# Kernel optimization log

Measured on AMD Instinct MI355X. Metric: run time of the kernel, lower is better.

The kernel has to match this reference:

```python
import jax, jax.numpy as jnp
import numpy as np

B, N, D = 8, 64, 512          # batch, latent tokens, token dim
C, H, W, P = 256, 128, 128, 36  # img feat channels/HW, sampling points
PG = 128                       # parameter-generator inner dim (0.25*D)
HEADS = 8                      # D // 64
TOT = C * C + P * P            # adaptive mixing param count per token


def _ln(x, g, b):
    m = x.mean(-1, keepdims=True)
    v = x.var(-1, keepdims=True)
    return (x - m) / jnp.sqrt(v + 1e-5) * g + b


def _gelu(x):
    return jax.nn.gelu(x, approximate=False)


def _grid_sample(img, grid):
    # img: (B,C,H,W); grid: (B,N,P,2) in [-1,1]; bilinear, border pad, align_corners=False
    Bi, Ci, Hi, Wi = img.shape
    x = ((grid[..., 0] + 1.0) * Wi - 1.0) * 0.5
    y = ((grid[..., 1] + 1.0) * Hi - 1.0) * 0.5
    x0 = jnp.floor(x)
    y0 = jnp.floor(y)
    wx = x - x0
    wy = y - y0
    x0i = jnp.clip(x0.astype(jnp.int32), 0, Wi - 1)
    x1i = jnp.clip(x0.astype(jnp.int32) + 1, 0, Wi - 1)
    y0i = jnp.clip(y0.astype(jnp.int32), 0, Hi - 1)
    y1i = jnp.clip(y0.astype(jnp.int32) + 1, 0, Hi - 1)
    imgt = img.transpose(0, 2, 3, 1)  # (B,H,W,C)
    bidx = jnp.arange(Bi)[:, None, None]
    v00 = imgt[bidx, y0i, x0i]  # (B,N,P,C)
    v01 = imgt[bidx, y0i, x1i]
    v10 = imgt[bidx, y1i, x0i]
    v11 = imgt[bidx, y1i, x1i]
    wx = wx[..., None]
    wy = wy[..., None]
    return (v00 * (1 - wx) * (1 - wy) + v01 * wx * (1 - wy)
            + v10 * (1 - wx) * wy + v11 * wx * wy)


def setup_inputs() -> dict:
    key = jax.random.key(0)
    ks = jax.random.split(key, 16)
    rn = lambda k, s, sc: jax.random.normal(k, s, jnp.float32) * sc
    tl = jax.random.uniform(ks[0], (B, N, 2), jnp.float32) * 0.5
    wh = 0.2 + jax.random.uniform(ks[1], (B, N, 2), jnp.float32) * 0.4
    return dict(
        token_embed=rn(ks[2], (B, N, D), 1.0),
        token_roi=jnp.concatenate([tl, tl + wh], axis=-1),
        img_feat=rn(ks[3], (B, C, H, W), 1.0),
        ln_off_g=jnp.ones(D), ln_off_b=jnp.zeros(D),
        w_off=rn(ks[4], (D, P * 2), D ** -0.5),
        roi_offset_bias=rn(ks[5], (P * 2,), 1.0),
        ln_pg_g=jnp.ones(D), ln_pg_b=jnp.zeros(D),
        w_pg1=rn(ks[6], (D, PG), D ** -0.5), b_pg1=jnp.zeros(PG),
        w_pg2=rn(ks[7], (PG, TOT), 0.02 * PG ** -0.5),
        b_pg2=rn(ks[8], (TOT,), 0.02),
        m_beta=jnp.zeros(C), s_beta=jnp.zeros(P),
        w_out=rn(ks[9], (P * C, D), (P * C) ** -0.5), b_out=jnp.zeros(D),
        ln1_g=jnp.ones(D), ln1_b=jnp.zeros(D),
        w_qkv=rn(ks[10], (D, 3 * D), D ** -0.5), b_qkv=jnp.zeros(3 * D),
        w_proj=rn(ks[11], (D, D), D ** -0.5), b_proj=jnp.zeros(D),
        ln2_g=jnp.ones(D), ln2_b=jnp.zeros(D),
        w_fc1=rn(ks[12], (D, 4 * D), D ** -0.5), b_fc1=jnp.zeros(4 * D),
        w_fc2=rn(ks[13], (4 * D, D), (4 * D) ** -0.5), b_fc2=jnp.zeros(D),
    )


def reference(token_embed, token_roi, img_feat,
              ln_off_g, ln_off_b, w_off, roi_offset_bias,
              ln_pg_g, ln_pg_b, w_pg1, b_pg1, w_pg2, b_pg2,
              m_beta, s_beta, w_out, b_out,
              ln1_g, ln1_b, w_qkv, b_qkv, w_proj, b_proj,
              ln2_g, ln2_b, w_fc1, b_fc1, w_fc2, b_fc2):
    Bq, Nq, Dm = token_embed.shape
    # --- OP.SAMPLING_M: offsets -> absolute points (n_heads=1) ---
    off = _ln(token_embed, ln_off_g, ln_off_b) @ w_off + roi_offset_bias  # (B,N,2P)
    off = off.reshape(Bq, Nq, 1, P, 2)
    mu = off.mean(-2, keepdims=True)
    sd = jnp.std(off, axis=-2, keepdims=True, ddof=1) + 1e-5  # unbiased, as torch.std
    off = (off - mu) / (3.0 * sd)
    xy = (token_roi[..., 2:] + token_roi[..., :2]) * 0.5
    wh = token_roi[..., 2:] - token_roi[..., :2]
    pts = xy[:, :, None, None, :] + off * wh[:, :, None, None, :]  # (B,N,1,P,2)
    grid = pts.reshape(Bq, Nq, P, 2) * 2.0 - 1.0
    sampled = _grid_sample(img_feat, grid)  # (B,N,P,C)
    # --- adaptive mixing (AdaMixer): per-token generated channel/spatial weights ---
    q = _ln(token_embed, ln_pg_g, ln_pg_b)
    params = (q @ w_pg1 + b_pg1) @ w_pg2 + b_pg2  # (B,N,TOT)
    cm = params[..., :C * C].reshape(Bq, Nq, C, C)
    sm = params[..., C * C:].reshape(Bq, Nq, P, P)
    h = _gelu(jnp.einsum('bnpc,bncd->bnpd', sampled, cm) + m_beta)
    h = _gelu(jnp.einsum('bnqp,bnpd->bnqd', sm, h) + s_beta[:, None])
    token_embed = token_embed + (h.reshape(Bq, Nq, P * C) @ w_out + b_out)
    # --- OP.ATTN ---
    x = _ln(token_embed, ln1_g, ln1_b)
    hd = Dm // HEADS
    qkv = (x @ w_qkv + b_qkv).reshape(Bq, Nq, 3, HEADS, hd)
    qh, kh, vh = qkv[:, :, 0], qkv[:, :, 1], qkv[:, :, 2]
    att = jax.nn.softmax(jnp.einsum('bqhd,bkhd->bhqk', qh, kh) * hd ** -0.5, axis=-1)
    o = jnp.einsum('bhqk,bkhd->bqhd', att, vh).reshape(Bq, Nq, Dm)
    token_embed = token_embed + (o @ w_proj + b_proj)
    # --- OP.MLP ---
    x = _ln(token_embed, ln2_g, ln2_b)
    token_embed = token_embed + (_gelu(x @ w_fc1 + b_fc1) @ w_fc2 + b_fc2)
    return token_embed
```

## Files before the change

kernel.cpp:

```cpp
#include <hip/hip_runtime.h>
#include <hip/hip_bf16.h>

typedef __hip_bfloat16 bf16;
typedef __attribute__((ext_vector_type(8))) short short8;
typedef __attribute__((ext_vector_type(4))) float f32x4;

#define NTOK 512
#define TOTC 66832
#define CM_SZ 65536

__device__ __forceinline__ float b2f(bf16 x) { return __bfloat162float(x); }
__device__ __forceinline__ bf16 f2b(float x) { return __float2bfloat16(x); }
__device__ __forceinline__ float gelu_f(float x) {
  return 0.5f * x * (1.0f + erff(x * 0.7071067811865476f));
}
__device__ __forceinline__ f32x4 mfma16(short8 a, short8 b, f32x4 c) {
  return __builtin_amdgcn_mfma_f32_16x16x32_bf16(a, b, c, 0, 0, 0);
}

__global__ __launch_bounds__(256) void k_transpose(const float* __restrict__ img,
                                                   bf16* __restrict__ imgT) {
  int b = blockIdx.y;
  int hw0 = blockIdx.x * 32;
  __shared__ float tile[256][33];
  int t = threadIdx.x;
  int hw = t & 31, c0 = t >> 5;
#pragma unroll 8
  for (int i = 0; i < 32; ++i) {
    int c = c0 + 8 * i;
    tile[c][hw] = img[((size_t)(b * 256 + c) << 14) + hw0 + hw];
  }
  __syncthreads();
#pragma unroll 8
  for (int i = 0; i < 32; ++i) {
    imgT[(((size_t)b << 14) + hw0 + i) * 256 + t] = f2b(tile[t][i]);
  }
}

__global__ __launch_bounds__(256) void k_prep(
    const float* __restrict__ te, const float* __restrict__ roi,
    const float* __restrict__ g_off, const float* __restrict__ b_off,
    const float* __restrict__ w_off, const float* __restrict__ off_bias,
    const float* __restrict__ g_pg, const float* __restrict__ b_pg,
    const float* __restrict__ w_pg1, const float* __restrict__ b_pg1,
    bf16* __restrict__ t_out, int* __restrict__ meta_i, float* __restrict__ meta_w) {
  int tok = blockIdx.x;
  int t = threadIdx.x, lane = t & 63, w = t >> 6;
  __shared__ float xo[512], xq[512], offb[72], red[4], wsum[4];
  size_t base = (size_t)tok * 512;
  float a0 = te[base + t];
  float a1 = te[base + t + 256];
  float s = a0 + a1;
#pragma unroll
  for (int o = 32; o; o >>= 1) s += __shfl_xor(s, o);
  if (lane == 0) wsum[w] = s;
  __syncthreads();
  float mean = (wsum[0] + wsum[1] + wsum[2] + wsum[3]) * (1.0f / 512.0f);
  float d0 = a0 - mean, d1 = a1 - mean;
  float ss = d0 * d0 + d1 * d1;
#pragma unroll
  for (int o = 32; o; o >>= 1) ss += __shfl_xor(ss, o);
  __syncthreads();
  if (lane == 0) wsum[w] = ss;
  __syncthreads();
  float var = (wsum[0] + wsum[1] + wsum[2] + wsum[3]) * (1.0f / 512.0f);
  float rstd = rsqrtf(var + 1e-5f);
  xo[t] = d0 * rstd * g_off[t] + b_off[t];
  xo[t + 256] = d1 * rstd * g_off[t + 256] + b_off[t + 256];
  xq[t] = d0 * rstd * g_pg[t] + b_pg[t];
  xq[t + 256] = d1 * rstd * g_pg[t + 256] + b_pg[t + 256];
  __syncthreads();
  if (t < 128) {
    float acc = b_pg1[t];
    for (int d = 0; d < 512; ++d) acc = fmaf(xq[d], w_pg1[d * 128 + t], acc);
    t_out[(size_t)tok * 128 + t] = f2b(acc);
  } else if (t < 200) {
    int j = t - 128;
    float acc = off_bias[j];
    for (int d = 0; d < 512; ++d) acc = fmaf(xo[d], w_off[d * 72 + j], acc);
    offb[j] = acc;
  }
  __syncthreads();
  if (t < 2) {
    float mu = 0.f;
    for (int p = 0; p < 36; ++p) mu += offb[p * 2 + t];
    mu *= (1.0f / 36.0f);
    float s2 = 0.f;
    for (int p = 0; p < 36; ++p) { float dd = offb[p * 2 + t] - mu; s2 += dd * dd; }
    float sd = sqrtf(s2 * (1.0f / 35.0f)) + 1e-5f;
    red[t] = mu;
    red[2 + t] = 1.0f / (3.0f * sd);
  }
  __syncthreads();
  if (t < 36) {
    int p = t;
    float r0 = roi[tok * 4 + 0], r1 = roi[tok * 4 + 1];
    float r2 = roi[tok * 4 + 2], r3 = roi[tok * 4 + 3];
    float cx = (r0 + r2) * 0.5f, cy = (r1 + r3) * 0.5f;
    float bw = r2 - r0, bh = r3 - r1;
    float ox = (offb[p * 2 + 0] - red[0]) * red[2];
    float oy = (offb[p * 2 + 1] - red[1]) * red[3];
    float fx = (cx + ox * bw) * 128.0f - 0.5f;
    float fy = (cy + oy * bh) * 128.0f - 0.5f;
    float x0f = floorf(fx), y0f = floorf(fy);
    float wx = fx - x0f, wy = fy - y0f;
    int x0 = min(max((int)x0f, 0), 127);
    int x1 = min(max((int)x0f + 1, 0), 127);
    int y0 = min(max((int)y0f, 0), 127);
    int y1 = min(max((int)y0f + 1, 0), 127);
    int ibase = (tok >> 6) * 16384;
    int mi = (tok * 36 + p) * 4;
    meta_i[mi + 0] = (ibase + y0 * 128 + x0) * 256;
    meta_i[mi + 1] = (ibase + y0 * 128 + x1) * 256;
    meta_i[mi + 2] = (ibase + y1 * 128 + x0) * 256;
    meta_i[mi + 3] = (ibase + y1 * 128 + x1) * 256;
    meta_w[mi + 0] = (1.f - wx) * (1.f - wy);
    meta_w[mi + 1] = wx * (1.f - wy);
    meta_w[mi + 2] = (1.f - wx) * wy;
    meta_w[mi + 3] = wx * wy;
  }
}

__global__ __launch_bounds__(256) void k_sample(const bf16* __restrict__ imgT,
                                                const int* __restrict__ meta_i,
                                                const float* __restrict__ meta_w,
                                                bf16* __restrict__ S) {
  int tok = blockIdx.x, t = threadIdx.x;
#pragma unroll 6
  for (int p = 0; p < 36; ++p) {
    int mi = (tok * 36 + p) * 4;
    int o00 = meta_i[mi + 0], o01 = meta_i[mi + 1], o10 = meta_i[mi + 2], o11 = meta_i[mi + 3];
    float w00 = meta_w[mi + 0], w01 = meta_w[mi + 1], w10 = meta_w[mi + 2], w11 = meta_w[mi + 3];
    float v = w00 * b2f(imgT[o00 + t]) + w01 * b2f(imgT[o01 + t]) +
              w10 * b2f(imgT[o10 + t]) + w11 * b2f(imgT[o11 + t]);
    S[((size_t)tok * 36 + p) * 256 + t] = f2b(v);
  }
}

__global__ __launch_bounds__(256) void k_wt(const float* __restrict__ w0, bf16* __restrict__ o0,
                                            const float* __restrict__ w1, bf16* __restrict__ o1,
                                            const float* __restrict__ w2, bf16* __restrict__ o2,
                                            const float* __restrict__ w3, bf16* __restrict__ o3,
                                            const float* __restrict__ w4, bf16* __restrict__ o4) {
  int b = blockIdx.x;
  const float* W;
  bf16* O;
  int K, N, loc;
  if (b < 4608) { W = w0; O = o0; K = 9216; N = 512; loc = b; }
  else if (b < 5376) { W = w1; O = o1; K = 512; N = 1536; loc = b - 4608; }
  else if (b < 5632) { W = w2; O = o2; K = 512; N = 512; loc = b - 5376; }
  else if (b < 6656) { W = w3; O = o3; K = 512; N = 2048; loc = b - 5632; }
  else { W = w4; O = o4; K = 2048; N = 512; loc = b - 6656; }
  int ntn = N >> 5;
  int nb = loc % ntn, kb = loc / ntn;
  int n0 = nb * 32, k0 = kb * 32;
  __shared__ float tl[32][33];
  int t = threadIdx.x, r = t >> 5, c = t & 31;
#pragma unroll
  for (int i = 0; i < 4; ++i)
    tl[r + 8 * i][c] = W[(size_t)(k0 + r + 8 * i) * N + n0 + c];
  __syncthreads();
#pragma unroll
  for (int i = 0; i < 4; ++i)
    O[(size_t)(n0 + r + 8 * i) * K + k0 + c] = f2b(tl[c][r + 8 * i]);
}

__global__ __launch_bounds__(256) void k_pg2_mfma(const bf16* __restrict__ tb16,
                                                  const float* __restrict__ w2,
                                                  const float* __restrict__ b2,
                                                  bf16* __restrict__ pchunk) {
  int n0 = blockIdx.x * 64;
  int row0 = blockIdx.y * 256;
  int t = threadIdx.x, lane = t & 63, w = t >> 6;
  int quad = lane >> 4, l16 = lane & 15;
  __shared__ bf16 BsT[64][136];
  {
    int nl = (t & 15) * 4, kk = t >> 4;
#pragma unroll
    for (int pass = 0; pass < 8; ++pass) {
      int k = kk + pass * 16;
      int n = n0 + nl;
      int nc = (n + 3 < TOTC) ? n : (TOTC - 4);
      const float4 v = *(const float4*)(w2 + (size_t)k * TOTC + nc);
      BsT[nl + 0][k] = f2b(v.x);
      BsT[nl + 1][k] = f2b(v.y);
      BsT[nl + 2][k] = f2b(v.z);
      BsT[nl + 3][k] = f2b(v.w);
    }
  }
  __syncthreads();
  f32x4 acc[4][4];
#pragma unroll
  for (int i = 0; i < 4; ++i)
#pragma unroll
    for (int j = 0; j < 4; ++j) acc[i][j] = (f32x4){0.f, 0.f, 0.f, 0.f};
  const bf16* Abase = tb16 + ((size_t)(row0 + w * 64 + l16)) * 128 + quad * 8;
#pragma unroll
  for (int ks = 0; ks < 4; ++ks) {
    short8 af[4], bff[4];
#pragma unroll
    for (int mt = 0; mt < 4; ++mt)
      af[mt] = *(const short8*)(Abase + mt * 16 * 128 + ks * 32);
#pragma unroll
    for (int nt = 0; nt < 4; ++nt)
      bff[nt] = *(const short8*)(&BsT[nt * 16 + l16][ks * 32 + quad * 8]);
#pragma unroll
    for (int mt = 0; mt < 4; ++mt)
#pragma unroll
      for (int nt = 0; nt < 4; ++nt)
        acc[mt][nt] = mfma16(af[mt], bff[nt], acc[mt][nt]);
  }
#pragma unroll
  for (int nt = 0; nt < 4; ++nt) {
    int col = n0 + nt * 16 + l16;
    if (col >= TOTC) continue;
    float bias = b2[col];
#pragma unroll
    for (int mt = 0; mt < 4; ++mt) {
      int r0 = row0 + w * 64 + mt * 16 + quad * 4;
#pragma unroll
      for (int r = 0; r < 4; ++r)
        pchunk[(size_t)(r0 + r) * TOTC + col] = f2b(acc[mt][nt][r] + bias);
    }
  }
}

__global__ __launch_bounds__(256) void k_mix3(const bf16* __restrict__ pchunk,
                                              const bf16* __restrict__ S,
                                              const float* __restrict__ m_beta,
                                              const float* __restrict__ s_beta,
                                              bf16* __restrict__ h2) {
  int tok = blockIdx.x, dh = blockIdx.y * 128;
  int t = threadIdx.x, lane = t & 63, w = t >> 6;
  int quad = lane >> 4, l16 = lane & 15;
  __shared__ bf16 h1T[128][72];
  __shared__ bf16 smS[48][72];
  __shared__ short cmw[4][32][40];
  for (int i = t; i < 1728; i += 256) ((unsigned*)smS)[i] = 0u;
  __syncthreads();
  const bf16* sm = pchunk + (size_t)tok * TOTC + CM_SZ;
  for (int i = t; i < 1296; i += 256) {
    int q = i / 36, p = i - q * 36;
    smS[q][p] = sm[i];
  }
  f32x4 acc[3][2];
#pragma unroll
  for (int i = 0; i < 3; ++i)
#pragma unroll
    for (int j = 0; j < 2; ++j) acc[i][j] = (f32x4){0.f, 0.f, 0.f, 0.f};
  const bf16* Sg = S + (size_t)tok * 9216;
  const bf16* Cg = pchunk + (size_t)tok * TOTC;
  int dw = w * 32;
  int c_l = lane & 31;
  int dtop = (lane >> 5) * 16;
  const bf16* src0 = Cg + (size_t)c_l * 256 + dh + dw + dtop;
  short8 v0 = *(const short8*)src0;
  short8 v1 = *(const short8*)(src0 + 8);
#pragma unroll
  for (int kc = 0; kc < 256; kc += 32) {
#pragma unroll
    for (int j = 0; j < 8; ++j) cmw[w][dtop + j][c_l] = v0[j];
#pragma unroll
    for (int j = 0; j < 8; ++j) cmw[w][dtop + 8 + j][c_l] = v1[j];
    short8 a[3];
#pragma unroll
    for (int mt = 0; mt < 3; ++mt)
      a[mt] = *(const short8*)(Sg + (size_t)(mt * 16 + l16) * 256 + kc + quad * 8);
    short8 v0n, v1n;
    if (kc < 224) {
      const bf16* srcn = Cg + (size_t)(kc + 32 + c_l) * 256 + dh + dw + dtop;
      v0n = *(const short8*)srcn;
      v1n = *(const short8*)(srcn + 8);
    }
    asm volatile("" ::: "memory");
    short8 bfr[2];
#pragma unroll
    for (int nt = 0; nt < 2; ++nt)
      bfr[nt] = *(const short8*)&cmw[w][nt * 16 + l16][quad * 8];
#pragma unroll
    for (int mt = 0; mt < 3; ++mt)
#pragma unroll
      for (int nt = 0; nt < 2; ++nt)
        acc[mt][nt] = mfma16(a[mt], bfr[nt], acc[mt][nt]);
    asm volatile("" ::: "memory");
    v0 = v0n;
    v1 = v1n;
  }
#pragma unroll
  for (int nt = 0; nt < 2; ++nt) {
    int dl = dw + nt * 16 + l16;
    float mb = m_beta[dh + dl];
#pragma unroll
    for (int mt = 0; mt < 3; ++mt)
#pragma unroll
      for (int r = 0; r < 4; ++r) {
        int p = mt * 16 + quad * 4 + r;
        if (p < 36) h1T[dl][p] = f2b(gelu_f(acc[mt][nt][r] + mb));
      }
  }
  for (int i = t; i < 128 * 28; i += 256) {
    int d = i / 28, p = 36 + i % 28;
    h1T[d][p] = (bf16)0.f;
  }
  __syncthreads();
  f32x4 acc2[3][2];
#pragma unroll
  for (int i = 0; i < 3; ++i)
#pragma unroll
    for (int j = 0; j < 2; ++j) acc2[i][j] = (f32x4){0.f, 0.f, 0.f, 0.f};
#pragma unroll
  for (int ks = 0; ks < 2; ++ks) {
    short8 a2[3], b2v[2];
#pragma unroll
    for (int mt = 0; mt < 3; ++mt)
      a2[mt] = *(const short8*)&smS[mt * 16 + l16][ks * 32 + quad * 8];
#pragma unroll
    for (int nt = 0; nt < 2; ++nt)
      b2v[nt] = *(const short8*)&h1T[dw + nt * 16 + l16][ks * 32 + quad * 8];
#pragma unroll
    for (int mt = 0; mt < 3; ++mt)
#pragma unroll
      for (int nt = 0; nt < 2; ++nt)
        acc2[mt][nt] = mfma16(a2[mt], b2v[nt], acc2[mt][nt]);
  }
  bf16* h2p = h2 + (size_t)tok * 9216 + dh;
#pragma unroll
  for (int mt = 0; mt < 3; ++mt)
#pragma unroll
    for (int r = 0; r < 4; ++r) {
      int q = mt * 16 + quad * 4 + r;
      if (q >= 36) continue;
      float sb = s_beta[q];
#pragma unroll
      for (int nt = 0; nt < 2; ++nt)
        h2p[q * 256 + dw + nt * 16 + l16] = f2b(gelu_f(acc2[mt][nt][r] + sb));
    }
}

__global__ __launch_bounds__(256) void k_gemm_bt(const bf16* __restrict__ A,
                                                 const bf16* __restrict__ BT,
                                                 float* __restrict__ part,
                                                 int M, int N, int K) {
  int nb = blockIdx.x, mb = blockIdx.y, ks = blockIdx.z;
  int kchunk = K / gridDim.z;
  int k0 = ks * kchunk;
  __shared__ bf16 As[64][72], Bs[64][72];
  int t = threadIdx.x, lane = t & 63, w = t >> 6;
  int quad = lane >> 4, l16 = lane & 15;
  int wm = (w >> 1) * 32, wn = (w & 1) * 32;
  int r = t >> 2, kk = (t & 3) * 16;
  f32x4 acc[2][2];
#pragma unroll
  for (int i = 0; i < 2; ++i)
#pragma unroll
    for (int j = 0; j < 2; ++j) acc[i][j] = (f32x4){0.f, 0.f, 0.f, 0.f};
  for (int kt = 0; kt < kchunk; kt += 64) {
    __syncthreads();
    const bf16* ga = A + (size_t)(mb * 64 + r) * K + k0 + kt + kk;
    *(short8*)&As[r][kk] = *(const short8*)ga;
    *(short8*)&As[r][kk + 8] = *(const short8*)(ga + 8);
    const bf16* gb = BT + (size_t)(nb * 64 + r) * K + k0 + kt + kk;
    *(short8*)&Bs[r][kk] = *(const short8*)gb;
    *(short8*)&Bs[r][kk + 8] = *(const short8*)(gb + 8);
    __syncthreads();
#pragma unroll
    for (int kss = 0; kss < 2; ++kss) {
      short8 af[2], bff[2];
#pragma unroll
      for (int mt = 0; mt < 2; ++mt)
        af[mt] = *(const short8*)&As[wm + mt * 16 + l16][kss * 32 + quad * 8];
#pragma unroll
      for (int nt = 0; nt < 2; ++nt)
        bff[nt] = *(const short8*)&Bs[wn + nt * 16 + l16][kss * 32 + quad * 8];
#pragma unroll
      for (int mt = 0; mt < 2; ++mt)
#pragma unroll
        for (int nt = 0; nt < 2; ++nt)
          acc[mt][nt] = mfma16(af[mt], bff[nt], acc[mt][nt]);
    }
  }
#pragma unroll
  for (int mt = 0; mt < 2; ++mt)
#pragma unroll
    for (int rr = 0; rr < 4; ++rr) {
      int m = mb * 64 + wm + mt * 16 + quad * 4 + rr;
#pragma unroll
      for (int nt = 0; nt < 2; ++nt) {
        int n = nb * 64 + wn + nt * 16 + l16;
        part[(size_t)ks * M * N + (size_t)m * N + n] = acc[mt][nt][rr];
      }
    }
}

__global__ __launch_bounds__(256) void k_epi(const float* __restrict__ part, int S_,
                                             int MN, int N, const float* __restrict__ bias,
                                             const float* __restrict__ resf, int do_gelu,
                                             float* __restrict__ outf, bf16* __restrict__ outh) {
  int idx = blockIdx.x * 256 + threadIdx.x;
  if (idx >= MN) return;
  int n = idx % N;
  float a = 0.f;
  for (int s = 0; s < S_; ++s) a += part[(size_t)s * MN + idx];
  a += bias[n];
  if (resf) a += resf[idx];
  if (do_gelu) a = gelu_f(a);
  if (outf) outf[idx] = a;
  if (outh) outh[idx] = f2b(a);
}

__global__ __launch_bounds__(256) void k_epi_ln(const float* __restrict__ part, int S_,
                                                const float* __restrict__ bias,
                                                const float* __restrict__ res,
                                                const float* __restrict__ g,
                                                const float* __restrict__ bvec,
                                                float* __restrict__ xout,
                                                bf16* __restrict__ lnout) {
  int tok = blockIdx.x, t = threadIdx.x, lane = t & 63, w = t >> 6;
  __shared__ float wsum[4];
  size_t base = (size_t)tok * 512;
  float a0 = bias[t] + res[base + t];
  float a1 = bias[t + 256] + res[base + t + 256];
  for (int sp = 0; sp < S_; ++sp) {
    const float* p = part + (size_t)sp * 262144 + base;
    a0 += p[t];
    a1 += p[t + 256];
  }
  xout[base + t] = a0;
  xout[base + t + 256] = a1;
  float s = a0 + a1;
#pragma unroll
  for (int o = 32; o; o >>= 1) s += __shfl_xor(s, o);
  if (lane == 0) wsum[w] = s;
  __syncthreads();
  float mean = (wsum[0] + wsum[1] + wsum[2] + wsum[3]) * (1.0f / 512.0f);
  float d0 = a0 - mean, d1 = a1 - mean;
  float ss = d0 * d0 + d1 * d1;
#pragma unroll
  for (int o = 32; o; o >>= 1) ss += __shfl_xor(ss, o);
  __syncthreads();
  if (lane == 0) wsum[w] = ss;
  __syncthreads();
  float var = (wsum[0] + wsum[1] + wsum[2] + wsum[3]) * (1.0f / 512.0f);
  float rstd = rsqrtf(var + 1e-5f);
  lnout[base + t] = f2b(d0 * rstd * g[t] + bvec[t]);
  lnout[base + t + 256] = f2b(d1 * rstd * g[t + 256] + bvec[t + 256]);
}

__global__ __launch_bounds__(256) void k_attn(const float* __restrict__ qkvf,
                                              bf16* __restrict__ obuf) {
  int b = blockIdx.x >> 3, h = blockIdx.x & 7;
  __shared__ float kT[64][65];
  __shared__ float vT[64][65];
  __shared__ float att[64][65];
  int t = threadIdx.x, lane = t & 63, w = t >> 6;
#pragma unroll
  for (int i = 0; i < 16; ++i) {
    int idx = t + i * 256;
    int j = idx >> 6, d = idx & 63;
    size_t tb = (size_t)(b * 64 + j) * 1536 + h * 64 + d;
    kT[j][d] = qkvf[tb + 512];
    vT[j][d] = qkvf[tb + 1024];
  }
  __syncthreads();
#pragma unroll 4
  for (int m = 0; m < 16; ++m) {
    int i = w * 16 + m;
    const float* qrow = &qkvf[(size_t)(b * 64 + i) * 1536 + h * 64];
    float s = 0.f;
    for (int d = 0; d < 64; ++d) s = fmaf(qrow[d], kT[lane][d], s);
    s *= 0.125f;
    float mx = s;
#pragma unroll
    for (int o = 32; o; o >>= 1) mx = fmaxf(mx, __shfl_xor(mx, o));
    float e = expf(s - mx);
    float sum = e;
#pragma unroll
    for (int o = 32; o; o >>= 1) sum += __shfl_xor(sum, o);
    att[i][lane] = e / sum;
  }
  __syncthreads();
#pragma unroll 4
  for (int m = 0; m < 16; ++m) {
    int i = w * 16 + m;
    float o = 0.f;
    for (int j = 0; j < 64; ++j) o = fmaf(att[i][j], vT[j][lane], o);
    obuf[(size_t)(b * 64 + i) * 512 + h * 64 + lane] = f2b(o);
  }
}

extern "C" void kernel_launch(void* const* d_in, const int* in_sizes, int n_in,
                              void* d_out, int out_size, void* d_ws, size_t ws_size,
                              hipStream_t stream) {
  const float* te = (const float*)d_in[0];
  const float* roi = (const float*)d_in[1];
  const float* img = (const float*)d_in[2];
  const float* ln_off_g = (const float*)d_in[3];
  const float* ln_off_b = (const float*)d_in[4];
  const float* w_off = (const float*)d_in[5];
  const float* off_bias = (const float*)d_in[6];
  const float* ln_pg_g = (const float*)d_in[7];
  const float* ln_pg_b = (const float*)d_in[8];
  const float* w_pg1 = (const float*)d_in[9];
  const float* b_pg1 = (const float*)d_in[10];
  const float* w_pg2 = (const float*)d_in[11];
  const float* b_pg2 = (const float*)d_in[12];
  const float* m_beta = (const float*)d_in[13];
  const float* s_beta = (const float*)d_in[14];
  const float* w_out = (const float*)d_in[15];
  const float* b_out = (const float*)d_in[16];
  const float* ln1_g = (const float*)d_in[17];
  const float* ln1_b = (const float*)d_in[18];
  const float* w_qkv = (const float*)d_in[19];
  const float* b_qkv = (const float*)d_in[20];
  const float* w_proj = (const float*)d_in[21];
  const float* b_proj = (const float*)d_in[22];
  const float* ln2_g = (const float*)d_in[23];
  const float* ln2_b = (const float*)d_in[24];
  const float* w_fc1 = (const float*)d_in[25];
  const float* b_fc1 = (const float*)d_in[26];
  const float* w_fc2 = (const float*)d_in[27];
  const float* b_fc2 = (const float*)d_in[28];

  char* ws = (char*)d_ws;
  bf16* imgT = (bf16*)ws;
  char* ov = ws;
  bf16* h2 = (bf16*)ov; ov += 9437184;
  float* part = (float*)ov; ov += 8388608;
  float* x1 = (float*)ov; ov += 1048576;
  float* xa = (float*)ov; ov += 1048576;
  float* qkvf = (float*)ov; ov += 3145728;
  bf16* ln1buf = (bf16*)ov; ov += 524288;
  bf16* ln2buf = (bf16*)ov; ov += 524288;
  bf16* obuf = (bf16*)ov; ov += 524288;
  bf16* hfc = (bf16*)ov; ov += 2097152;
  char* tail = ws + 67108864;
  bf16* Sbuf = (bf16*)tail; tail += 9437184;
  bf16* tb16 = (bf16*)tail; tail += 131072;
  int* meta_i = (int*)tail; tail += 294912;
  float* meta_w = (float*)tail; tail += 294912;
  bf16* pchunk = (bf16*)tail; tail += (size_t)NTOK * TOTC * 2;
  bf16* w_outT = (bf16*)tail; tail += 9437184;
  bf16* w_qkvT = (bf16*)tail; tail += 1572864;
  bf16* w_projT = (bf16*)tail; tail += 524288;
  bf16* w_fc1T = (bf16*)tail; tail += 2097152;
  bf16* w_fc2T = (bf16*)tail; tail += 2097152;
  (void)ws_size;

  k_transpose<<<dim3(512, 8), 256, 0, stream>>>(img, imgT);
  k_prep<<<512, 256, 0, stream>>>(te, roi, ln_off_g, ln_off_b, w_off, off_bias,
                                  ln_pg_g, ln_pg_b, w_pg1, b_pg1, tb16, meta_i, meta_w);
  k_sample<<<512, 256, 0, stream>>>(imgT, meta_i, meta_w, Sbuf);
  k_wt<<<7680, 256, 0, stream>>>(w_out, w_outT, w_qkv, w_qkvT, w_proj, w_projT,
                                 w_fc1, w_fc1T, w_fc2, w_fc2T);
  k_pg2_mfma<<<dim3(1045, 2), 256, 0, stream>>>(tb16, w_pg2, b_pg2, pchunk);
  k_mix3<<<dim3(512, 2), 256, 0, stream>>>(pchunk, Sbuf, m_beta, s_beta, h2);

  k_gemm_bt<<<dim3(8, 8, 8), 256, 0, stream>>>(h2, w_outT, part, 512, 512, 9216);
  k_epi_ln<<<512, 256, 0, stream>>>(part, 8, b_out, te, ln1_g, ln1_b, x1, ln1buf);

  k_gemm_bt<<<dim3(24, 8, 2), 256, 0, stream>>>(ln1buf, w_qkvT, part, 512, 1536, 512);
  k_epi<<<3072, 256, 0, stream>>>(part, 2, 512 * 1536, 1536, b_qkv, nullptr, 0, qkvf, nullptr);
  k_attn<<<64, 256, 0, stream>>>(qkvf, obuf);
  k_gemm_bt<<<dim3(8, 8, 4), 256, 0, stream>>>(obuf, w_projT, part, 512, 512, 512);
  k_epi_ln<<<512, 256, 0, stream>>>(part, 4, b_proj, x1, ln2_g, ln2_b, xa, ln2buf);

  k_gemm_bt<<<dim3(32, 8, 2), 256, 0, stream>>>(ln2buf, w_fc1T, part, 512, 2048, 512);
  k_epi<<<4096, 256, 0, stream>>>(part, 2, 512 * 2048, 2048, b_fc1, nullptr, 1, nullptr, hfc);
  k_gemm_bt<<<dim3(8, 8, 4), 256, 0, stream>>>(hfc, w_fc2T, part, 512, 512, 2048);
  k_epi<<<1024, 256, 0, stream>>>(part, 4, 512 * 512, 512, b_fc2, xa, 0, (float*)d_out, nullptr);
}
```

Baseline: 537.0 us.

## Merge prep kernels into fewer launches and fuse GEMM epilogues

Merges the prep, image-transpose and weight-transpose kernels into one block-indexed launch, and co-schedules the bilinear sampling blocks with the pg2 MFMA GEMM in a second launch. Replaces the split-K GEMM plus separate epilogue for QKV and FC1 with a single GEMM that applies bias and GELU directly. Splits attention across query chunks to get more blocks. The aim is fewer kernel launches, no partial-sum round trips to memory, and better occupancy. The trade-off is a larger shared-memory footprint for the merged kernel and no split-K parallelism for the fused GEMMs.

```diff
diff --git a/kernel.cpp b/kernel.cpp
--- a/kernel.cpp
+++ b/kernel.cpp
@@ -18,209 +18,215 @@
   return __builtin_amdgcn_mfma_f32_16x16x32_bf16(a, b, c, 0, 0, 0);
 }
 
-__global__ __launch_bounds__(256) void k_transpose(const float* __restrict__ img,
-                                                   bf16* __restrict__ imgT) {
-  int b = blockIdx.y;
-  int hw0 = blockIdx.x * 32;
-  __shared__ float tile[256][33];
-  int t = threadIdx.x;
-  int hw = t & 31, c0 = t >> 5;
-#pragma unroll 8
-  for (int i = 0; i < 32; ++i) {
-    int c = c0 + 8 * i;
-    tile[c][hw] = img[((size_t)(b * 256 + c) << 14) + hw0 + hw];
-  }
-  __syncthreads();
-#pragma unroll 8
-  for (int i = 0; i < 32; ++i) {
-    imgT[(((size_t)b << 14) + hw0 + i) * 256 + t] = f2b(tile[t][i]);
-  }
-}
-
-__global__ __launch_bounds__(256) void k_prep(
+__global__ __launch_bounds__(256) void k_head(
     const float* __restrict__ te, const float* __restrict__ roi,
     const float* __restrict__ g_off, const float* __restrict__ b_off,
     const float* __restrict__ w_off, const float* __restrict__ off_bias,
     const float* __restrict__ g_pg, const float* __restrict__ b_pg,
     const float* __restrict__ w_pg1, const float* __restrict__ b_pg1,
-    bf16* __restrict__ t_out, int* __restrict__ meta_i, float* __restrict__ meta_w) {
-  int tok = blockIdx.x;
-  int t = threadIdx.x, lane = t & 63, w = t >> 6;
-  __shared__ float xo[512], xq[512], offb[72], red[4], wsum[4];
-  size_t base = (size_t)tok * 512;
-  float a0 = te[base + t];
-  float a1 = te[base + t + 256];
-  float s = a0 + a1;
-#pragma unroll
-  for (int o = 32; o; o >>= 1) s += __shfl_xor(s, o);
-  if (lane == 0) wsum[w] = s;
-  __syncthreads();
-  float mean = (wsum[0] + wsum[1] + wsum[2] + wsum[3]) * (1.0f / 512.0f);
-  float d0 = a0 - mean, d1 = a1 - mean;
-  float ss = d0 * d0 + d1 * d1;
-#pragma unroll
-  for (int o = 32; o; o >>= 1) ss += __shfl_xor(ss, o);
-  __syncthreads();
-  if (lane == 0) wsum[w] = ss;
-  __syncthreads();
-  float var = (wsum[0] + wsum[1] + wsum[2] + wsum[3]) * (1.0f / 512.0f);
-  float rstd = rsqrtf(var + 1e-5f);
-  xo[t] = d0 * rstd * g_off[t] + b_off[t];
-  xo[t + 256] = d1 * rstd * g_off[t + 256] + b_off[t + 256];
-  xq[t] = d0 * rstd * g_pg[t] + b_pg[t];
-  xq[t + 256] = d1 * rstd * g_pg[t + 256] + b_pg[t + 256];
-  __syncthreads();
-  if (t < 128) {
-    float acc = b_pg1[t];
-    for (int d = 0; d < 512; ++d) acc = fmaf(xq[d], w_pg1[d * 128 + t], acc);
-    t_out[(size_t)tok * 128 + t] = f2b(acc);
-  } else if (t < 200) {
-    int j = t - 128;
-    float acc = off_bias[j];
-    for (int d = 0; d < 512; ++d) acc = fmaf(xo[d], w_off[d * 72 + j], acc);
-    offb[j] = acc;
-  }
-  __syncthreads();
-  if (t < 2) {
-    float mu = 0.f;
-    for (int p = 0; p < 36; ++p) mu += offb[p * 2 + t];
-    mu *= (1.0f / 36.0f);
-    float s2 = 0.f;
-    for (int p = 0; p < 36; ++p) { float dd = offb[p * 2 + t] - mu; s2 += dd * dd; }
-    float sd = sqrtf(s2 * (1.0f / 35.0f)) + 1e-5f;
-    red[t] = mu;
-    red[2 + t] = 1.0f / (3.0f * sd);
-  }
-  __syncthreads();
-  if (t < 36) {
-    int p = t;
-    float r0 = roi[tok * 4 + 0], r1 = roi[tok * 4 + 1];
-    float r2 = roi[tok * 4 + 2], r3 = roi[tok * 4 + 3];
-    float cx = (r0 + r2) * 0.5f, cy = (r1 + r3) * 0.5f;
-    float bw = r2 - r0, bh = r3 - r1;
-    float ox = (offb[p * 2 + 0] - red[0]) * red[2];
-    float oy = (offb[p * 2 + 1] - red[1]) * red[3];
-    float fx = (cx + ox * bw) * 128.0f - 0.5f;
-    float fy = (cy + oy * bh) * 128.0f - 0.5f;
-    float x0f = floorf(fx), y0f = floorf(fy);
-    float wx = fx - x0f, wy = fy - y0f;
-    int x0 = min(max((int)x0f, 0), 127);
-    int x1 = min(max((int)x0f + 1, 0), 127);
-    int y0 = min(max((int)y0f, 0), 127);
-    int y1 = min(max((int)y0f + 1, 0), 127);
-    int ibase = (tok >> 6) * 16384;
-    int mi = (tok * 36 + p) * 4;
-    meta_i[mi + 0] = (ibase + y0 * 128 + x0) * 256;
-    meta_i[mi + 1] = (ibase + y0 * 128 + x1) * 256;
-    meta_i[mi + 2] = (ibase + y1 * 128 + x0) * 256;
-    meta_i[mi + 3] = (ibase + y1 * 128 + x1) * 256;
-    meta_w[mi + 0] = (1.f - wx) * (1.f - wy);
-    meta_w[mi + 1] = wx * (1.f - wy);
-    meta_w[mi + 2] = (1.f - wx) * wy;
-    meta_w[mi + 3] = wx * wy;
-  }
-}
-
-__global__ __launch_bounds__(256) void k_sample(const bf16* __restrict__ imgT,
-                                                const int* __restrict__ meta_i,
-                                                const float* __restrict__ meta_w,
-                                                bf16* __restrict__ S) {
-  int tok = blockIdx.x, t = threadIdx.x;
+    bf16* __restrict__ t_out, int* __restrict__ meta_i, float* __restrict__ meta_w,
+    const float* __restrict__ img, bf16* __restrict__ imgT,
+    const float* __restrict__ w0, bf16* __restrict__ o0,
+    const float* __restrict__ w1, bf16* __restrict__ o1,
+    const float* __restrict__ w2, bf16* __restrict__ o2,
+    const float* __restrict__ w3, bf16* __restrict__ o3,
+    const float* __restrict__ w4, bf16* __restrict__ o4) {
+  __shared__ float smem[8448];
+  int blk = blockIdx.x;
+  int t = threadIdx.x;
+  if (blk < 512) {
+    int tok = blk;
+    int lane = t & 63, w = t >> 6;
+    float* xo = smem;
+    float* xq = smem + 512;
+    float* offb = smem + 1024;
+    float* red = smem + 1096;
+    float* wsum = smem + 1100;
+    size_t base = (size_t)tok * 512;
+    float a0 = te[base + t];
+    float a1 = te[base + t + 256];
+    float s = a0 + a1;
+#pragma unroll
+    for (int o = 32; o; o >>= 1) s += __shfl_xor(s, o);
+    if (lane == 0) wsum[w] = s;
+    __syncthreads();
+    float mean = (wsum[0] + wsum[1] + wsum[2] + wsum[3]) * (1.0f / 512.0f);
+    float d0 = a0 - mean, d1 = a1 - mean;
+    float ss = d0 * d0 + d1 * d1;
+#pragma unroll
+    for (int o = 32; o; o >>= 1) ss += __shfl_xor(ss, o);
+    __syncthreads();
+    if (lane == 0) wsum[w] = ss;
+    __syncthreads();
+    float var = (wsum[0] + wsum[1] + wsum[2] + wsum[3]) * (1.0f / 512.0f);
+    float rstd = rsqrtf(var + 1e-5f);
+    xo[t] = d0 * rstd * g_off[t] + b_off[t];
+    xo[t + 256] = d1 * rstd * g_off[t + 256] + b_off[t + 256];
+    xq[t] = d0 * rstd * g_pg[t] + b_pg[t];
+    xq[t + 256] = d1 * rstd * g_pg[t + 256] + b_pg[t + 256];
+    __syncthreads();
+    if (t < 128) {
+      float acc = b_pg1[t];
+      for (int d = 0; d < 512; ++d) acc = fmaf(xq[d], w_pg1[d * 128 + t], acc);
+      t_out[(size_t)tok * 128 + t] = f2b(acc);
+    } else if (t < 200) {
+      int j = t - 128;
+      float acc = off_bias[j];
+      for (int d = 0; d < 512; ++d) acc = fmaf(xo[d], w_off[d * 72 + j], acc);
+      offb[j] = acc;
+    }
+    __syncthreads();
+    if (t < 2) {
+      float mu = 0.f;
+      for (int p = 0; p < 36; ++p) mu += offb[p * 2 + t];
+      mu *= (1.0f / 36.0f);
+      float s2 = 0.f;
+      for (int p = 0; p < 36; ++p) { float dd = offb[p * 2 + t] - mu; s2 += dd * dd; }
+      float sd = sqrtf(s2 * (1.0f / 35.0f)) + 1e-5f;
+      red[t] = mu;
+      red[2 + t] = 1.0f / (3.0f * sd);
+    }
+    __syncthreads();
+    if (t < 36) {
+      int p = t;
+      float r0 = roi[tok * 4 + 0], r1 = roi[tok * 4 + 1];
+      float r2 = roi[tok * 4 + 2], r3 = roi[tok * 4 + 3];
+      float cx = (r0 + r2) * 0.5f, cy = (r1 + r3) * 0.5f;
+      float bw = r2 - r0, bh = r3 - r1;
+      float ox = (offb[p * 2 + 0] - red[0]) * red[2];
+      float oy = (offb[p * 2 + 1] - red[1]) * red[3];
+      float fx = (cx + ox * bw) * 128.0f - 0.5f;
+      float fy = (cy + oy * bh) * 128.0f - 0.5f;
+      float x0f = floorf(fx), y0f = floorf(fy);
+      float wx = fx - x0f, wy = fy - y0f;
+      int x0 = min(max((int)x0f, 0), 127);
+      int x1 = min(max((int)x0f + 1, 0), 127);
+      int y0 = min(max((int)y0f, 0), 127);
+      int y1 = min(max((int)y0f + 1, 0), 127);
+      int ibase = (tok >> 6) * 16384;
+      int mi = (tok * 36 + p) * 4;
+      meta_i[mi + 0] = (ibase + y0 * 128 + x0) * 256;
+      meta_i[mi + 1] = (ibase + y0 * 128 + x1) * 256;
+      meta_i[mi + 2] = (ibase + y1 * 128 + x0) * 256;
+      meta_i[mi + 3] = (ibase + y1 * 128 + x1) * 256;
+      meta_w[mi + 0] = (1.f - wx) * (1.f - wy);
+      meta_w[mi + 1] = wx * (1.f - wy);
+      meta_w[mi + 2] = (1.f - wx) * wy;
+      meta_w[mi + 3] = wx * wy;
+    }
+  } else if (blk < 4608) {
+    int bb = blk - 512;
+    int b = bb >> 9;
+    int hw0 = (bb & 511) * 32;
+    float (*tile)[33] = (float(*)[33])smem;
+    int hw = t & 31, c0 = t >> 5;
+#pragma unroll 8
+    for (int i = 0; i < 32; ++i) {
+      int c = c0 + 8 * i;
+      tile[c][hw] = img[((size_t)(b * 256 + c) << 14) + hw0 + hw];
+    }
+    __syncthreads();
+#pragma unroll 8
+    for (int i = 0; i < 32; ++i) {
+      imgT[(((size_t)b << 14) + hw0 + i) * 256 + t] = f2b(tile[t][i]);
+    }
+  } else {
+    int b = blk - 4608;
+    const float* W;
+    bf16* O;
+    int K, N, loc;
+    if (b < 4608) { W = w0; O = o0; K = 9216; N = 512; loc = b; }
+    else if (b < 5376) { W = w1; O = o1; K = 512; N = 1536; loc = b - 4608; }
+    else if (b < 5632) { W = w2; O = o2; K = 512; N = 512; loc = b - 5376; }
+    else if (b < 6656) { W = w3; O = o3; K = 512; N = 2048; loc = b - 5632; }
+    else { W = w4; O = o4; K = 2048; N = 512; loc = b - 6656; }
+    int ntn = N >> 5;
+    int nb = loc % ntn, kb = loc / ntn;
+    int n0 = nb * 32, k0 = kb * 32;
+    float (*tl)[33] = (float(*)[33])smem;
+    int r = t >> 5, c = t & 31;
+#pragma unroll
+    for (int i = 0; i < 4; ++i)
+      tl[r + 8 * i][c] = W[(size_t)(k0 + r + 8 * i) * N + n0 + c];
+    __syncthreads();
+#pragma unroll
+    for (int i = 0; i < 4; ++i)
+      O[(size_t)(n0 + r + 8 * i) * K + k0 + c] = f2b(tl[c][r + 8 * i]);
+  }
+}
+
+__global__ __launch_bounds__(256) void k_samp_pg2(
+    const bf16* __restrict__ tb16, const float* __restrict__ w2,
+    const float* __restrict__ b2, bf16* __restrict__ pchunk,
+    const bf16* __restrict__ imgT, const int* __restrict__ meta_i,
+    const float* __restrict__ meta_w, bf16* __restrict__ S) {
+  __shared__ bf16 BsT[64][136];
+  int blk = blockIdx.x;
+  int t = threadIdx.x;
+  if (blk < 2090) {
+    int n0 = (blk % 1045) * 64;
+    int row0 = (blk / 1045) * 256;
+    int lane = t & 63, w = t >> 6;
+    int quad = lane >> 4, l16 = lane & 15;
+    {
+      int nl = (t & 15) * 4, kk = t >> 4;
+#pragma unroll
+      for (int pass = 0; pass < 8; ++pass) {
+        int k = kk + pass * 16;
+        int n = n0 + nl;
+        int nc = (n + 3 < TOTC) ? n : (TOTC - 4);
+        const float4 v = *(const float4*)(w2 + (size_t)k * TOTC + nc);
+        BsT[nl + 0][k] = f2b(v.x);
+        BsT[nl + 1][k] = f2b(v.y);
+        BsT[nl + 2][k] = f2b(v.z);
+        BsT[nl + 3][k] = f2b(v.w);
+      }
+    }
+    __syncthreads();
+    f32x4 acc[4][4];
+#pragma unroll
+    for (int i = 0; i < 4; ++i)
+#pragma unroll
+      for (int j = 0; j < 4; ++j) acc[i][j] = (f32x4){0.f, 0.f, 0.f, 0.f};
+    const bf16* Abase = tb16 + ((size_t)(row0 + w * 64 + l16)) * 128 + quad * 8;
+#pragma unroll
+    for (int ks = 0; ks < 4; ++ks) {
+      short8 af[4], bff[4];
+#pragma unroll
+      for (int mt = 0; mt < 4; ++mt)
+        af[mt] = *(const short8*)(Abase + mt * 16 * 128 + ks * 32);
+#pragma unroll
+      for (int nt = 0; nt < 4; ++nt)
+        bff[nt] = *(const short8*)(&BsT[nt * 16 + l16][ks * 32 + quad * 8]);
+#pragma unroll
+      for (int mt = 0; mt < 4; ++mt)
+#pragma unroll
+        for (int nt = 0; nt < 4; ++nt)
+          acc[mt][nt] = mfma16(af[mt], bff[nt], acc[mt][nt]);
+    }
+#pragma unroll
+    for (int nt = 0; nt < 4; ++nt) {
+      int col = n0 + nt * 16 + l16;
+      if (col >= TOTC) continue;
+      float bias = b2[col];
+#pragma unroll
+      for (int mt = 0; mt < 4; ++mt) {
+        int r0 = row0 + w * 64 + mt * 16 + quad * 4;
+#pragma unroll
+        for (int r = 0; r < 4; ++r)
+          pchunk[(size_t)(r0 + r) * TOTC + col] = f2b(acc[mt][nt][r] + bias);
+      }
+    }
+  } else {
+    int tok = blk - 2090;
 #pragma unroll 6
-  for (int p = 0; p < 36; ++p) {
-    int mi = (tok * 36 + p) * 4;
-    int o00 = meta_i[mi + 0], o01 = meta_i[mi + 1], o10 = meta_i[mi + 2], o11 = meta_i[mi + 3];
-    float w00 = meta_w[mi + 0], w01 = meta_w[mi + 1], w10 = meta_w[mi + 2], w11 = meta_w[mi + 3];
-    float v = w00 * b2f(imgT[o00 + t]) + w01 * b2f(imgT[o01 + t]) +
-              w10 * b2f(imgT[o10 + t]) + w11 * b2f(imgT[o11 + t]);
-    S[((size_t)tok * 36 + p) * 256 + t] = f2b(v);
-  }
-}
-
-__global__ __launch_bounds__(256) void k_wt(const float* __restrict__ w0, bf16* __restrict__ o0,
-                                            const float* __restrict__ w1, bf16* __restrict__ o1,
-                                            const float* __restrict__ w2, bf16* __restrict__ o2,
-                                            const float* __restrict__ w3, bf16* __restrict__ o3,
-                                            const float* __restrict__ w4, bf16* __restrict__ o4) {
-  int b = blockIdx.x;
-  const float* W;
-  bf16* O;
-  int K, N, loc;
-  if (b < 4608) { W = w0; O = o0; K = 9216; N = 512; loc = b; }
-  else if (b < 5376) { W = w1; O = o1; K = 512; N = 1536; loc = b - 4608; }
-  else if (b < 5632) { W = w2; O = o2; K = 512; N = 512; loc = b - 5376; }
-  else if (b < 6656) { W = w3; O = o3; K = 512; N = 2048; loc = b - 5632; }
-  else { W = w4; O = o4; K = 2048; N = 512; loc = b - 6656; }
-  int ntn = N >> 5;
-  int nb = loc % ntn, kb = loc / ntn;
-  int n0 = nb * 32, k0 = kb * 32;
-  __shared__ float tl[32][33];
-  int t = threadIdx.x, r = t >> 5, c = t & 31;
-#pragma unroll
-  for (int i = 0; i < 4; ++i)
-    tl[r + 8 * i][c] = W[(size_t)(k0 + r + 8 * i) * N + n0 + c];
-  __syncthreads();
-#pragma unroll
-  for (int i = 0; i < 4; ++i)
-    O[(size_t)(n0 + r + 8 * i) * K + k0 + c] = f2b(tl[c][r + 8 * i]);
-}
-
-__global__ __launch_bounds__(256) void k_pg2_mfma(const bf16* __restrict__ tb16,
-                                                  const float* __restrict__ w2,
-                                                  const float* __restrict__ b2,
-                                                  bf16* __restrict__ pchunk) {
-  int n0 = blockIdx.x * 64;
-  int row0 = blockIdx.y * 256;
-  int t = threadIdx.x, lane = t & 63, w = t >> 6;
-  int quad = lane >> 4, l16 = lane & 15;
-  __shared__ bf16 BsT[64][136];
-  {
-    int nl = (t & 15) * 4, kk = t >> 4;
-#pragma unroll
-    for (int pass = 0; pass < 8; ++pass) {
-      int k = kk + pass * 16;
-      int n = n0 + nl;
-      int nc = (n + 3 < TOTC) ? n : (TOTC - 4);
-      const float4 v = *(const float4*)(w2 + (size_t)k * TOTC + nc);
-      BsT[nl + 0][k] = f2b(v.x);
-      BsT[nl + 1][k] = f2b(v.y);
-      BsT[nl + 2][k] = f2b(v.z);
-      BsT[nl + 3][k] = f2b(v.w);
-    }
-  }
-  __syncthreads();
-  f32x4 acc[4][4];
-#pragma unroll
-  for (int i = 0; i < 4; ++i)
-#pragma unroll
-    for (int j = 0; j < 4; ++j) acc[i][j] = (f32x4){0.f, 0.f, 0.f, 0.f};
-  const bf16* Abase = tb16 + ((size_t)(row0 + w * 64 + l16)) * 128 + quad * 8;
-#pragma unroll
-  for (int ks = 0; ks < 4; ++ks) {
-    short8 af[4], bff[4];
-#pragma unroll
-    for (int mt = 0; mt < 4; ++mt)
-      af[mt] = *(const short8*)(Abase + mt * 16 * 128 + ks * 32);
-#pragma unroll
-    for (int nt = 0; nt < 4; ++nt)
-      bff[nt] = *(const short8*)(&BsT[nt * 16 + l16][ks * 32 + quad * 8]);
-#pragma unroll
-    for (int mt = 0; mt < 4; ++mt)
-#pragma unroll
-      for (int nt = 0; nt < 4; ++nt)
-        acc[mt][nt] = mfma16(af[mt], bff[nt], acc[mt][nt]);
-  }
-#pragma unroll
-  for (int nt = 0; nt < 4; ++nt) {
-    int col = n0 + nt * 16 + l16;
-    if (col >= TOTC) continue;
-    float bias = b2[col];
-#pragma unroll
-    for (int mt = 0; mt < 4; ++mt) {
-      int r0 = row0 + w * 64 + mt * 16 + quad * 4;
-#pragma unroll
-      for (int r = 0; r < 4; ++r)
-        pchunk[(size_t)(r0 + r) * TOTC + col] = f2b(acc[mt][nt][r] + bias);
+    for (int p = 0; p < 36; ++p) {
+      int mi = (tok * 36 + p) * 4;
+      int o00 = meta_i[mi + 0], o01 = meta_i[mi + 1], o10 = meta_i[mi + 2], o11 = meta_i[mi + 3];
+      float w00 = meta_w[mi + 0], w01 = meta_w[mi + 1], w10 = meta_w[mi + 2], w11 = meta_w[mi + 3];
+      float v = w00 * b2f(imgT[o00 + t]) + w01 * b2f(imgT[o01 + t]) +
+                w10 * b2f(imgT[o10 + t]) + w11 * b2f(imgT[o11 + t]);
+      S[((size_t)tok * 36 + p) * 256 + t] = f2b(v);
     }
   }
 }
@@ -392,6 +398,64 @@
     }
 }
 
+__global__ __launch_bounds__(256) void k_gemm_ep(const bf16* __restrict__ A,
+                                                 const bf16* __restrict__ BT,
+                                                 const float* __restrict__ bias,
+                                                 int M, int N, int K, int do_gelu,
+                                                 float* __restrict__ outf,
+                                                 bf16* __restrict__ outh) {
+  int nb = blockIdx.x, mb = blockIdx.y;
+  __shared__ bf16 As[64][72], Bs[64][72];
+  int t = threadIdx.x, lane = t & 63, w = t >> 6;
+  int quad = lane >> 4, l16 = lane & 15;
+  int wm = (w >> 1) * 32, wn = (w & 1) * 32;
+  int r = t >> 2, kk = (t & 3) * 16;
+  f32x4 acc[2][2];
+#pragma unroll
+  for (int i = 0; i < 2; ++i)
+#pragma unroll
+    for (int j = 0; j < 2; ++j) acc[i][j] = (f32x4){0.f, 0.f, 0.f, 0.f};
+  for (int kt = 0; kt < K; kt += 64) {
+    __syncthreads();
+    const bf16* ga = A + (size_t)(mb * 64 + r) * K + kt + kk;
+    *(short8*)&As[r][kk] = *(const short8*)ga;
+    *(short8*)&As[r][kk + 8] = *(const short8*)(ga + 8);
+    const bf16* gb = BT + (size_t)(nb * 64 + r) * K + kt + kk;
+    *(short8*)&Bs[r][kk] = *(const short8*)gb;
+    *(short8*)&Bs[r][kk + 8] = *(const short8*)(gb + 8);
+    __syncthreads();
+#pragma unroll
+    for (int kss = 0; kss < 2; ++kss) {
+      short8 af[2], bff[2];
+#pragma unroll
+      for (int mt = 0; mt < 2; ++mt)
+        af[mt] = *(const short8*)&As[wm + mt * 16 + l16][kss * 32 + quad * 8];
+#pragma unroll
+      for (int nt = 0; nt < 2; ++nt)
+        bff[nt] = *(const short8*)&Bs[wn + nt * 16 + l16][kss * 32 + quad * 8];
+#pragma unroll
+      for (int mt = 0; mt < 2; ++mt)
+#pragma unroll
+        for (int nt = 0; nt < 2; ++nt)
+          acc[mt][nt] = mfma16(af[mt], bff[nt], acc[mt][nt]);
+    }
+  }
+#pragma unroll
+  for (int mt = 0; mt < 2; ++mt)
+#pragma unroll
+    for (int rr = 0; rr < 4; ++rr) {
+      int m = mb * 64 + wm + mt * 16 + quad * 4 + rr;
+#pragma unroll
+      for (int nt = 0; nt < 2; ++nt) {
+        int n = nb * 64 + wn + nt * 16 + l16;
+        float a = acc[mt][nt][rr] + bias[n];
+        if (do_gelu) a = gelu_f(a);
+        if (outf) outf[(size_t)m * N + n] = a;
+        else outh[(size_t)m * N + n] = f2b(a);
+      }
+    }
+}
+
 __global__ __launch_bounds__(256) void k_epi(const float* __restrict__ part, int S_,
                                              int MN, int N, const float* __restrict__ bias,
                                              const float* __restrict__ resf, int do_gelu,
@@ -449,9 +513,10 @@
 __global__ __launch_bounds__(256) void k_attn(const float* __restrict__ qkvf,
                                               bf16* __restrict__ obuf) {
   int b = blockIdx.x >> 3, h = blockIdx.x & 7;
+  int q0 = blockIdx.y * 16;
   __shared__ float kT[64][65];
   __shared__ float vT[64][65];
-  __shared__ float att[64][65];
+  __shared__ float att[16][65];
   int t = threadIdx.x, lane = t & 63, w = t >> 6;
 #pragma unroll
   for (int i = 0; i < 16; ++i) {
@@ -462,9 +527,10 @@
     vT[j][d] = qkvf[tb + 1024];
   }
   __syncthreads();
-#pragma unroll 4
-  for (int m = 0; m < 16; ++m) {
-    int i = w * 16 + m;
+#pragma unroll
+  for (int m = 0; m < 4; ++m) {
+    int il = w * 4 + m;
+    int i = q0 + il;
     const float* qrow = &qkvf[(size_t)(b * 64 + i) * 1536 + h * 64];
     float s = 0.f;
     for (int d = 0; d < 64; ++d) s = fmaf(qrow[d], kT[lane][d], s);
@@ -476,14 +542,15 @@
     float sum = e;
 #pragma unroll
     for (int o = 32; o; o >>= 1) sum += __shfl_xor(sum, o);
-    att[i][lane] = e / sum;
+    att[il][lane] = e / sum;
   }
   __syncthreads();
-#pragma unroll 4
-  for (int m = 0; m < 16; ++m) {
-    int i = w * 16 + m;
+#pragma unroll
+  for (int m = 0; m < 4; ++m) {
+    int il = w * 4 + m;
+    int i = q0 + il;
     float o = 0.f;
-    for (int j = 0; j < 64; ++j) o = fmaf(att[i][j], vT[j][lane], o);
+    for (int j = 0; j < 64; ++j) o = fmaf(att[il][j], vT[j][lane], o);
     obuf[(size_t)(b * 64 + i) * 512 + h * 64 + lane] = f2b(o);
   }
 }
@@ -546,26 +613,26 @@
   bf16* w_fc2T = (bf16*)tail; tail += 2097152;
   (void)ws_size;
 
-  k_transpose<<<dim3(512, 8), 256, 0, stream>>>(img, imgT);
-  k_prep<<<512, 256, 0, stream>>>(te, roi, ln_off_g, ln_off_b, w_off, off_bias,
-                                  ln_pg_g, ln_pg_b, w_pg1, b_pg1, tb16, meta_i, meta_w);
-  k_sample<<<512, 256, 0, stream>>>(imgT, meta_i, meta_w, Sbuf);
-  k_wt<<<7680, 256, 0, stream>>>(w_out, w_outT, w_qkv, w_qkvT, w_proj, w_projT,
-                                 w_fc1, w_fc1T, w_fc2, w_fc2T);
-  k_pg2_mfma<<<dim3(1045, 2), 256, 0, stream>>>(tb16, w_pg2, b_pg2, pchunk);
+  k_head<<<12288, 256, 0, stream>>>(te, roi, ln_off_g, ln_off_b, w_off, off_bias,
+                                    ln_pg_g, ln_pg_b, w_pg1, b_pg1, tb16, meta_i, meta_w,
+                                    img, imgT,
+                                    w_out, w_outT, w_qkv, w_qkvT, w_proj, w_projT,
+                                    w_fc1, w_fc1T, w_fc2, w_fc2T);
+  k_samp_pg2<<<2602, 256, 0, stream>>>(tb16, w_pg2, b_pg2, pchunk,
+                                       imgT, meta_i, meta_w, Sbuf);
   k_mix3<<<dim3(512, 2), 256, 0, stream>>>(pchunk, Sbuf, m_beta, s_beta, h2);
 
   k_gemm_bt<<<dim3(8, 8, 8), 256, 0, stream>>>(h2, w_outT, part, 512, 512, 9216);
   k_epi_ln<<<512, 256, 0, stream>>>(part, 8, b_out, te, ln1_g, ln1_b, x1, ln1buf);
 
-  k_gemm_bt<<<dim3(24, 8, 2), 256, 0, stream>>>(ln1buf, w_qkvT, part, 512, 1536, 512);
-  k_epi<<<3072, 256, 0, stream>>>(part, 2, 512 * 1536, 1536, b_qkv, nullptr, 0, qkvf, nullptr);
-  k_attn<<<64, 256, 0, stream>>>(qkvf, obuf);
+  k_gemm_ep<<<dim3(24, 8), 256, 0, stream>>>(ln1buf, w_qkvT, b_qkv, 512, 1536, 512, 0,
+                                             qkvf, nullptr);
+  k_attn<<<dim3(64, 4), 256, 0, stream>>>(qkvf, obuf);
   k_gemm_bt<<<dim3(8, 8, 4), 256, 0, stream>>>(obuf, w_projT, part, 512, 512, 512);
   k_epi_ln<<<512, 256, 0, stream>>>(part, 4, b_proj, x1, ln2_g, ln2_b, xa, ln2buf);
 
-  k_gemm_bt<<<dim3(32, 8, 2), 256, 0, stream>>>(ln2buf, w_fc1T, part, 512, 2048, 512);
-  k_epi<<<4096, 256, 0, stream>>>(part, 2, 512 * 2048, 2048, b_fc1, nullptr, 1, nullptr, hfc);
+  k_gemm_ep<<<dim3(32, 8), 256, 0, stream>>>(ln2buf, w_fc1T, b_fc1, 512, 2048, 512, 1,
+                                             nullptr, hfc);
   k_gemm_bt<<<dim3(8, 8, 4), 256, 0, stream>>>(hfc, w_fc2T, part, 512, 512, 2048);
   k_epi<<<1024, 256, 0, stream>>>(part, 4, 512 * 512, 512, b_fc2, xa, 0, (float*)d_out, nullptr);
 }
```

Result: faster. 482.5 us (-10.2%).
